# Kernel optimization log

Hardware: AMD Instinct MI355X
Metric: run time of the kernel (lower is better)

Reference implementation:

```python
import jax, jax.numpy as jnp
import numpy as np

NUM_HEADS = 6
HEAD_SIZE = 64
N_EMBD = 384


def setup_inputs() -> dict:
    key = jax.random.key(0)
    ks = jax.random.split(key, 6)
    B, T, C = 4, 2048, N_EMBD
    D = NUM_HEADS * HEAD_SIZE  # 384
    x = jax.random.normal(ks[0], (B, T, C), dtype=jnp.float32)
    scale = 1.0 / np.sqrt(C)
    Wq = jax.random.normal(ks[1], (C, D), dtype=jnp.float32) * scale
    Wk = jax.random.normal(ks[2], (C, D), dtype=jnp.float32) * scale
    Wv = jax.random.normal(ks[3], (C, D), dtype=jnp.float32) * scale
    Wp = jax.random.normal(ks[4], (D, N_EMBD), dtype=jnp.float32) * scale
    bp = jnp.zeros((N_EMBD,), dtype=jnp.float32)
    return {"x": x, "Wq": Wq, "Wk": Wk, "Wv": Wv, "Wp": Wp, "bp": bp}


def reference(x, Wq, Wk, Wv, Wp, bp):
    B, T, C = x.shape
    H, Dh = NUM_HEADS, HEAD_SIZE
    # QKV projections (no bias), split into heads: [B, H, T, Dh]
    q = (x @ Wq).reshape(B, T, H, Dh).transpose(0, 2, 1, 3)
    k = (x @ Wk).reshape(B, T, H, Dh).transpose(0, 2, 1, 3)
    v = (x @ Wv).reshape(B, T, H, Dh).transpose(0, 2, 1, 3)
    # scaled dot-product scores [B, H, T, T]
    scores = jnp.einsum("bhqd,bhkd->bhqk", q, k) / jnp.sqrt(jnp.float32(Dh))
    causal = jnp.tril(jnp.ones((T, T), dtype=bool))
    scores = jnp.where(causal, scores, jnp.float32(-1e9))
    attn = jax.nn.softmax(scores, axis=-1)
    # dropout is identity at inference (Keras Dropout inactive outside training)
    out = jnp.einsum("bhqk,bhkd->bhqd", attn, v)
    out = out.transpose(0, 2, 1, 3).reshape(B, T, H * Dh)
    return out @ Wp + bp
```

## Files before the change

kernel.cpp:

```cpp
#include <hip/hip_runtime.h>
#include <hip/hip_bf16.h>

typedef __bf16 bf16x8 __attribute__((ext_vector_type(8)));
typedef float floatx4 __attribute__((ext_vector_type(4)));
typedef unsigned short us4 __attribute__((ext_vector_type(4)));
typedef unsigned short us8 __attribute__((ext_vector_type(8)));
typedef unsigned short ushort_t;

#define MFMA(a,b,c) __builtin_amdgcn_mfma_f32_16x16x32_bf16((a),(b),(c),0,0,0)


__device__ __forceinline__ ushort_t f2bf(float f){
  unsigned u = __builtin_bit_cast(unsigned, f);
  u = u + 0x7fffu + ((u>>16)&1u);
  return (ushort_t)(u>>16);
}

__device__ __forceinline__ us4 pack4(float4 a){
  us4 o;
  o[0]=f2bf(a.x); o[1]=f2bf(a.y); o[2]=f2bf(a.z); o[3]=f2bf(a.w);
  return o;
}

__device__ __forceinline__ us4 cvt4(floatx4 v){
  union { us4 s; __hip_bfloat162 h[2]; } u;
  float2 t;
  t.x=v[0]; t.y=v[1]; u.h[0]=__float22bfloat162_rn(t);
  t.x=v[2]; t.y=v[3]; u.h[1]=__float22bfloat162_rn(t);
  return u.s;
}

__global__ __launch_bounds__(256) void prep(
    const float* __restrict__ x,
    const float* __restrict__ w0, const float* __restrict__ w1,
    const float* __restrict__ w2, const float* __restrict__ w3,
    ushort_t* __restrict__ xb,
    ushort_t* __restrict__ wt_qkv, ushort_t* __restrict__ wt_p){
  __shared__ ushort_t tile[64][65];
  int bx = blockIdx.x;
  if (bx < 3072){
    int i = (bx*256 + threadIdx.x)*4;
    int row = i/384, col = i - row*384;
    float4 v = *(const float4*)(x + i);
    us4 o;
    o[0]=f2bf(v.x); o[1]=f2bf(v.y); o[2]=f2bf(v.z); o[3]=f2bf(v.w);
    *(us4*)(xb + ((row>>4)*48 + (col>>3))*128 + (row&15)*8 + (col&7)) = o;
    return;
  }
  int t6 = bx - 3072;
  int z = t6/36, rem = t6%36, by = rem/6, bxx = rem%6;
  const float* src; ushort_t* dst;
  if      (z==0){ src=w0; dst=wt_qkv;             }
  else if (z==1){ src=w1; dst=wt_qkv + 147456;    }
  else if (z==2){ src=w2; dst=wt_qkv + 2*147456;  }
  else          { src=w3; dst=wt_p;               }
  int r0 = by*64, c0 = bxx*64;
  int t = threadIdx.x, r = t>>2, cs = (t&3)*16;
  #pragma unroll
  for (int i=0;i<16;i++) tile[r][cs+i] = f2bf(src[(r0+r)*384 + c0+cs+i]);
  __syncthreads();
  int n = c0 + r, t16n = n>>4, rn = n&15;
  int k0 = r0 + cs;
  #pragma unroll
  for (int i=0;i<16;i++){
    int k = k0 + i;
    dst[(t16n*48 + (k>>3))*128 + rn*8 + (k&7)] = tile[cs+i][r];
  }
}

__global__ __launch_bounds__(64) void qkv_gemm(
    const ushort_t* __restrict__ x, const ushort_t* __restrict__ wt,
    ushort_t* __restrict__ qb, ushort_t* __restrict__ kb, ushort_t* __restrict__ vtb){
  __shared__ ushort_t tr[16*72];
  int lane = threadIdx.x&63, l15 = lane&15, quad = lane>>4;
  int mb = blockIdx.x*64, mt = blockIdx.x*4;
  int z  = blockIdx.y/6;
  int nt16 = (blockIdx.y - z*6)*4;
  int n0 = nt16*16;
  const ushort_t* wbase = wt + z*147456;
  floatx4 acc[4][4];
  #pragma unroll
  for (int qs=0;qs<4;qs++)
    #pragma unroll
    for (int nt=0;nt<4;nt++) acc[qs][nt]=(floatx4){0,0,0,0};
  #pragma unroll
  for (int kt=0; kt<12; kt++){
    bf16x8 a[4], b[4];
    #pragma unroll
    for (int qs=0; qs<4; qs++)
      a[qs] = *(const bf16x8*)(x + ((mt+qs)*48 + kt*4+quad)*128 + l15*8);
    #pragma unroll
    for (int nt=0; nt<4; nt++)
      b[nt] = *(const bf16x8*)(wbase + ((nt16+nt)*48 + kt*4+quad)*128 + l15*8);
    #pragma unroll
    for (int qs=0; qs<4; qs++)
      #pragma unroll
      for (int nt=0; nt<4; nt++)
        acc[qs][nt] = MFMA(a[qs], b[nt], acc[qs][nt]);
  }
  int h = n0>>6;
  if (z == 2){
    #pragma unroll
    for (int qs=0; qs<4; qs++){
      int rbase = mb + qs*16 + quad*4;
      int b_ = rbase >> 11, rr = rbase & 2047;
      int ct = rr>>3, e0 = rr&7;
      #pragma unroll
      for (int nt=0; nt<4; nt++){
        float4 v; v.x=acc[qs][nt][0]; v.y=acc[qs][nt][1];
                  v.z=acc[qs][nt][2]; v.w=acc[qs][nt][3];
        *(us4*)(vtb + ((b_*6+h)*1024 + nt*256 + ct)*128 + l15*8 + e0) = pack4(v);
      }
    }
  } else {
    float qscale = (z==0) ? 0.18033688011112042f : 1.0f;
    ushort_t* dstp = (z==0) ? qb : kb;
    #pragma unroll
    for (int qs=0; qs<4; qs++){
      int rbase = mb + qs*16;
      int b_ = rbase>>11, t16 = (rbase&2047)>>4;
      #pragma unroll
      for (int nt=0; nt<4; nt++)
        #pragma unroll
        for (int j=0; j<4; j++)
          tr[(quad*4+j)*72 + nt*16 + l15] = f2bf(acc[qs][nt][j]*qscale);
      us8 v0 = *(const us8*)(&tr[l15*72 + quad*8]);
      us8 v1 = *(const us8*)(&tr[l15*72 + (quad+4)*8]);
      int hbase = (b_*6+h)*1024 + t16*8;
      *(us8*)(dstp + (hbase + quad  )*128 + l15*8) = v0;
      *(us8*)(dstp + (hbase + quad+4)*128 + l15*8) = v1;
    }
  }
}

__device__ __forceinline__ void subtile(
    const bf16x8 (&kf)[4][2], const bf16x8 (&vf)[4][2], bf16x8 ones,
    bf16x8 qf0, bf16x8 qf1,
    floatx4 (&o4)[4], floatx4& lsum,
    ushort_t* pwv, int qg, int kv0, bool diag, int l15, int quad){
  floatx4 s[4];
  #pragma unroll
  for (int nt=0; nt<4; nt++){
    floatx4 z = {0,0,0,0};
    z = MFMA(kf[nt][0], qf0, z);
    z = MFMA(kf[nt][1], qf1, z);
    s[nt] = z;
  }
  ushort_t* prow = pwv + l15*72;
  if (diag){
    #pragma unroll
    for (int nt=0; nt<4; nt++){
      floatx4 p;
      #pragma unroll
      for (int r=0;r<4;r++){
        int kvg = kv0 + nt*16 + quad*4 + r;
        float sv = (kvg > qg) ? -1e30f : s[nt][r];
        p[r] = exp2f(sv);
      }
      *(us4*)(prow + nt*16 + quad*4) = cvt4(p);
    }
  } else {
    #pragma unroll
    for (int nt=0; nt<4; nt++){
      floatx4 p;
      #pragma unroll
      for (int r=0;r<4;r++) p[r] = exp2f(s[nt][r]);
      *(us4*)(prow + nt*16 + quad*4) = cvt4(p);
    }
  }
  bf16x8 pa0 = *(const bf16x8*)(prow + quad*8);
  bf16x8 pa1 = *(const bf16x8*)(prow + 32 + quad*8);
  #pragma unroll
  for (int nt=0; nt<4; nt++){
    o4[nt] = MFMA(pa0, vf[nt][0], o4[nt]);
    o4[nt] = MFMA(pa1, vf[nt][1], o4[nt]);
  }
  lsum = MFMA(pa0, ones, lsum);
  lsum = MFMA(pa1, ones, lsum);
}

__global__ __launch_bounds__(256,2) void attn(
    const ushort_t* __restrict__ qb, const ushort_t* __restrict__ kb,
    const ushort_t* __restrict__ vtb, ushort_t* __restrict__ ob){
  __shared__ float smem[4608];
  int bx = blockIdx.x;
  int hb = bx % 24;
  int p  = bx / 24;
  int tA = p, tB = 63 - p;
  int ktA = tA >> 1, ktB = tB >> 1;
  int h = hb % 6, b = hb / 6;
  int lane = threadIdx.x&63, w = threadIdx.x>>6, l15 = lane&15, quad = lane>>4;
  const ushort_t* qbase = qb  + (b*6+h)*131072;
  const ushort_t* kbase = kb  + (b*6+h)*131072;
  const ushort_t* vbase = vtb + (b*6+h)*131072;

  bf16x8 qfA[2][2], qfB[2][2];
  #pragma unroll
  for (int s=0; s<2; s++){
    const ushort_t* qpA = qbase + ((tA*2+s)*8 + quad)*128 + l15*8;
    qfA[s][0] = *(const bf16x8*)(qpA);
    qfA[s][1] = *(const bf16x8*)(qpA + 512);
    const ushort_t* qpB = qbase + ((tB*2+s)*8 + quad)*128 + l15*8;
    qfB[s][0] = *(const bf16x8*)(qpB);
    qfB[s][1] = *(const bf16x8*)(qpB + 512);
  }
  union { us8 u; bf16x8 v; } onesu;
  #pragma unroll
  for (int i=0;i<8;i++) onesu.u[i] = 0x3F80;
  bf16x8 ones = onesu.v;

  floatx4 oA[2][4], oB[2][4];
  floatx4 lsA[2], lsB[2];
  #pragma unroll
  for (int s=0;s<2;s++){
    lsA[s] = (floatx4){0,0,0,0};
    lsB[s] = (floatx4){0,0,0,0};
    #pragma unroll
    for (int i=0;i<4;i++){ oA[s][i]=(floatx4){0,0,0,0}; oB[s][i]=(floatx4){0,0,0,0}; }
  }

  ushort_t* pw = (ushort_t*)smem + w*1152;
  int qA0 = tA*32, qB0 = tB*32;

  for (int kt=w; kt<=ktB; kt+=4){
    int kv0 = kt*64;
    bf16x8 kf[4][2], vf[4][2];
    #pragma unroll
    for (int nt=0; nt<4; nt++){
      const ushort_t* kp = kbase + ((kt*4+nt)*8 + quad)*128 + l15*8;
      kf[nt][0] = *(const bf16x8*)(kp);
      kf[nt][1] = *(const bf16x8*)(kp + 512);
      const ushort_t* vp = vbase + (nt*256 + kt*8 + quad)*128 + l15*8;
      vf[nt][0] = *(const bf16x8*)(vp);
      vf[nt][1] = *(const bf16x8*)(vp + 512);
    }
    bool diagB = (kt == ktB);
    subtile(kf,vf,ones,qfB[0][0],qfB[0][1], oB[0], lsB[0], pw, qB0   +l15, kv0, diagB, l15, quad);
    subtile(kf,vf,ones,qfB[1][0],qfB[1][1], oB[1], lsB[1], pw, qB0+16+l15, kv0, diagB, l15, quad);
    if (kt <= ktA){
      bool diagA = (kt == ktA);
      subtile(kf,vf,ones,qfA[0][0],qfA[0][1], oA[0], lsA[0], pw, qA0   +l15, kv0, diagA, l15, quad);
      subtile(kf,vf,ones,qfA[1][0],qfA[1][1], oA[1], lsA[1], pw, qA0+16+l15, kv0, diagA, l15, quad);
    }
  }

  float* lsh = smem + 4352;
  if (l15==0){
    #pragma unroll
    for (int j=0;j<4;j++){
      lsh[w*64 +      quad*4 + j] = lsA[0][j];
      lsh[w*64 + 16 + quad*4 + j] = lsA[1][j];
      lsh[w*64 + 32 + quad*4 + j] = lsB[0][j];
      lsh[w*64 + 48 + quad*4 + j] = lsB[1][j];
    }
  }

  auto do_chunk = [&](const floatx4 (&oc)[4], int c, int grc){
    __syncthreads();
    #pragma unroll
    for (int j=0;j<4;j++){
      int r16 = quad*4 + j;
      #pragma unroll
      for (int nt=0;nt<4;nt++)
        smem[w*1088 + r16*68 + nt*16 + l15] = oc[nt][j];
    }
    __syncthreads();
    #pragma unroll
    for (int jj=0;jj<4;jj++){
      int r16 = w*4 + jj;
      float l = lsh[c*16+r16] + lsh[64+c*16+r16]
              + lsh[128+c*16+r16] + lsh[192+c*16+r16];
      float acc = smem[r16*68+lane] + smem[1088 + r16*68+lane]
                + smem[2176 + r16*68+lane] + smem[3264 + r16*68+lane];
      ob[((b*128 + grc)*48 + h*8 + (lane>>3))*128 + r16*8 + (lane&7)]
          = f2bf(acc/l);
    }
  };
  do_chunk(oA[0], 0, tA*2);
  do_chunk(oA[1], 1, tA*2+1);
  do_chunk(oB[0], 2, tB*2);
  do_chunk(oB[1], 3, tB*2+1);
}

__global__ __launch_bounds__(64) void proj_gemm(
    const ushort_t* __restrict__ a, const ushort_t* __restrict__ wpt,
    const float* __restrict__ bp, float* __restrict__ out){
  int lane = threadIdx.x&63, l15 = lane&15, quad = lane>>4;
  int mb = blockIdx.x*64, mt = blockIdx.x*4;
  int nb = blockIdx.y*64, nt16 = blockIdx.y*4;
  floatx4 acc[4][4];
  #pragma unroll
  for (int qs=0;qs<4;qs++)
    #pragma unroll
    for (int nt=0;nt<4;nt++) acc[qs][nt]=(floatx4){0,0,0,0};
  #pragma unroll
  for (int kt=0; kt<12; kt++){
    bf16x8 av[4], bv[4];
    #pragma unroll
    for (int qs=0; qs<4; qs++)
      av[qs] = *(const bf16x8*)(a + ((mt+qs)*48 + kt*4+quad)*128 + l15*8);
    #pragma unroll
    for (int nt=0; nt<4; nt++)
      bv[nt] = *(const bf16x8*)(wpt + ((nt16+nt)*48 + kt*4+quad)*128 + l15*8);
    #pragma unroll
    for (int qs=0; qs<4; qs++)
      #pragma unroll
      for (int nt=0; nt<4; nt++)
        acc[qs][nt] = MFMA(av[qs], bv[nt], acc[qs][nt]);
  }
  #pragma unroll
  for (int qs=0; qs<4; qs++){
    #pragma unroll
    for (int nt=0; nt<4; nt++){
      int c = nb + nt*16 + l15;
      float bias = bp[c];
      #pragma unroll
      for (int j=0; j<4; j++){
        int r = mb + qs*16 + quad*4 + j;
        out[r*384 + c] = acc[qs][nt][j] + bias;
      }
    }
  }
}

extern "C" void kernel_launch(void* const* d_in, const int* in_sizes, int n_in,
                              void* d_out, int out_size, void* d_ws, size_t ws_size,
                              hipStream_t stream){
  const float* x  = (const float*)d_in[0];
  const float* Wq = (const float*)d_in[1];
  const float* Wk = (const float*)d_in[2];
  const float* Wv = (const float*)d_in[3];
  const float* Wp = (const float*)d_in[4];
  const float* bp = (const float*)d_in[5];
  float* out = (float*)d_out;

  ushort_t* xb  = (ushort_t*)d_ws;
  ushort_t* wt  = xb  + 8192*384;
  ushort_t* wpt = wt  + 1152*384;
  ushort_t* qb  = wpt + 384*384;
  ushort_t* kb  = qb  + 8192*384;
  ushort_t* vtb = kb  + 8192*384;
  ushort_t* ab  = vtb + 8192*384;

  prep     <<<dim3(3216),   256, 0, stream>>>(x,Wq,Wk,Wv,Wp,xb,wt,wpt);
  qkv_gemm <<<dim3(128,18), 64,  0, stream>>>(xb, wt, qb, kb, vtb);
  attn     <<<dim3(768),    256, 0, stream>>>(qb, kb, vtb, ab);
  proj_gemm<<<dim3(128,6),  64,  0, stream>>>(ab, wpt, bp, out);
}
```

Measured before the change: 132.8 us.

## Prefetch next K/V tile and interleave score/PV stages across subtiles

Splits the per-subtile work into separate score and PV phases using four LDS probability slices per wave, so score MFMAs for one query subtile can overlap PV MFMAs of another. K and V fragments for the next kv tile are loaded into registers during the current iteration (software pipelining) to hide global memory latency. This quadruples per-wave LDS staging and adds register pressure from double-buffered fragments, which may reduce occupancy or cause spills.

Result: no change. 131.5 us, median of 3 (-1.0%).

```diff
diff --git a/kernel.cpp b/kernel.cpp
--- a/kernel.cpp
+++ b/kernel.cpp
@@ -133,11 +133,9 @@
   }
 }
 
-__device__ __forceinline__ void subtile(
-    const bf16x8 (&kf)[4][2], const bf16x8 (&vf)[4][2], bf16x8 ones,
-    bf16x8 qf0, bf16x8 qf1,
-    floatx4 (&o4)[4], floatx4& lsum,
-    ushort_t* pwv, int qg, int kv0, bool diag, int l15, int quad){
+__device__ __forceinline__ void score(
+    const bf16x8 (&kf)[4][2], bf16x8 qf0, bf16x8 qf1,
+    ushort_t* slice, int qg, int kv0, bool diag, int l15, int quad){
   floatx4 s[4];
   #pragma unroll
   for (int nt=0; nt<4; nt++){
@@ -146,7 +144,7 @@
     z = MFMA(kf[nt][1], qf1, z);
     s[nt] = z;
   }
-  ushort_t* prow = pwv + l15*72;
+  ushort_t* prow = slice + l15*72;
   if (diag){
     #pragma unroll
     for (int nt=0; nt<4; nt++){
@@ -168,6 +166,12 @@
       *(us4*)(prow + nt*16 + quad*4) = cvt4(p);
     }
   }
+}
+
+__device__ __forceinline__ void pv(
+    const bf16x8 (&vf)[4][2], bf16x8 ones, ushort_t* slice,
+    floatx4 (&o4)[4], floatx4& lsum, int l15, int quad){
+  ushort_t* prow = slice + l15*72;
   bf16x8 pa0 = *(const bf16x8*)(prow + quad*8);
   bf16x8 pa1 = *(const bf16x8*)(prow + 32 + quad*8);
   #pragma unroll
@@ -182,7 +186,7 @@
 __global__ __launch_bounds__(256,2) void attn(
     const ushort_t* __restrict__ qb, const ushort_t* __restrict__ kb,
     const ushort_t* __restrict__ vtb, ushort_t* __restrict__ ob){
-  __shared__ float smem[4608];
+  __shared__ float smem[9472];
   int bx = blockIdx.x;
   int hb = bx % 24;
   int p  = bx / 24;
@@ -219,32 +223,62 @@
     for (int i=0;i<4;i++){ oA[s][i]=(floatx4){0,0,0,0}; oB[s][i]=(floatx4){0,0,0,0}; }
   }
 
-  ushort_t* pw = (ushort_t*)smem + w*1152;
+  ushort_t* s0 = (ushort_t*)smem + w*4608;
+  ushort_t* s1 = s0 + 1152;
+  ushort_t* s2 = s0 + 2304;
+  ushort_t* s3 = s0 + 3456;
   int qA0 = tA*32, qB0 = tB*32;
+
+  auto LOADK = [&](int t, bf16x8 (&kf_)[4][2]){
+    #pragma unroll
+    for (int nt=0; nt<4; nt++){
+      const ushort_t* kp = kbase + ((t*4+nt)*8 + quad)*128 + l15*8;
+      kf_[nt][0] = *(const bf16x8*)(kp);
+      kf_[nt][1] = *(const bf16x8*)(kp + 512);
+    }
+  };
+  auto LOADV = [&](int t, bf16x8 (&vf_)[4][2]){
+    #pragma unroll
+    for (int nt=0; nt<4; nt++){
+      const ushort_t* vp = vbase + (nt*256 + t*8 + quad)*128 + l15*8;
+      vf_[nt][0] = *(const bf16x8*)(vp);
+      vf_[nt][1] = *(const bf16x8*)(vp + 512);
+    }
+  };
+
+  bf16x8 kf[4][2], vf[4][2];
+  LOADK(w, kf); LOADV(w, vf);
 
   for (int kt=w; kt<=ktB; kt+=4){
     int kv0 = kt*64;
-    bf16x8 kf[4][2], vf[4][2];
-    #pragma unroll
-    for (int nt=0; nt<4; nt++){
-      const ushort_t* kp = kbase + ((kt*4+nt)*8 + quad)*128 + l15*8;
-      kf[nt][0] = *(const bf16x8*)(kp);
-      kf[nt][1] = *(const bf16x8*)(kp + 512);
-      const ushort_t* vp = vbase + (nt*256 + kt*8 + quad)*128 + l15*8;
-      vf[nt][0] = *(const bf16x8*)(vp);
-      vf[nt][1] = *(const bf16x8*)(vp + 512);
-    }
+    int ktn = (kt+4 <= ktB) ? kt+4 : ktB;
     bool diagB = (kt == ktB);
-    subtile(kf,vf,ones,qfB[0][0],qfB[0][1], oB[0], lsB[0], pw, qB0   +l15, kv0, diagB, l15, quad);
-    subtile(kf,vf,ones,qfB[1][0],qfB[1][1], oB[1], lsB[1], pw, qB0+16+l15, kv0, diagB, l15, quad);
+    bf16x8 kn[4][2], vn[4][2];
+    score(kf, qfB[0][0],qfB[0][1], s0, qB0   +l15, kv0, diagB, l15, quad);
+    score(kf, qfB[1][0],qfB[1][1], s1, qB0+16+l15, kv0, diagB, l15, quad);
+    pv(vf, ones, s0, oB[0], lsB[0], l15, quad);
     if (kt <= ktA){
       bool diagA = (kt == ktA);
-      subtile(kf,vf,ones,qfA[0][0],qfA[0][1], oA[0], lsA[0], pw, qA0   +l15, kv0, diagA, l15, quad);
-      subtile(kf,vf,ones,qfA[1][0],qfA[1][1], oA[1], lsA[1], pw, qA0+16+l15, kv0, diagA, l15, quad);
-    }
-  }
-
-  float* lsh = smem + 4352;
+      score(kf, qfA[0][0],qfA[0][1], s2, qA0   +l15, kv0, diagA, l15, quad);
+      pv(vf, ones, s1, oB[1], lsB[1], l15, quad);
+      score(kf, qfA[1][0],qfA[1][1], s3, qA0+16+l15, kv0, diagA, l15, quad);
+      LOADK(ktn, kn);
+      pv(vf, ones, s2, oA[0], lsA[0], l15, quad);
+      pv(vf, ones, s3, oA[1], lsA[1], l15, quad);
+      LOADV(ktn, vn);
+    } else {
+      pv(vf, ones, s1, oB[1], lsB[1], l15, quad);
+      LOADK(ktn, kn);
+      LOADV(ktn, vn);
+    }
+    #pragma unroll
+    for (int nt=0; nt<4; nt++){
+      kf[nt][0]=kn[nt][0]; kf[nt][1]=kn[nt][1];
+      vf[nt][0]=vn[nt][0]; vf[nt][1]=vn[nt][1];
+    }
+  }
+
+  float* lsh = smem + 9216;
   if (l15==0){
     #pragma unroll
     for (int j=0;j<4;j++){
```

## Give each attention block one query tile and split score/PV into separate stages

Applied to the files above, without the earlier changes.

Before, each attention block handled a pair of query tiles (p and 63-p) to balance the causal workload. Now each block handles a single 32-row query tile, the grid doubles to 1536 blocks, and blocks are ordered from the longest tile to the shortest. The per-subtile routine is split into a score step and a PV step, and each 16-row half gets its own LDS slice so both score computations can be issued before the PV MFMAs, giving the scheduler more independent work. The cost is that K/V fragments are loaded twice as often across the grid, per-block work is uneven, and LDS use per block grows.

After: 131.9 us. No clear change (-0.6%).

```diff
diff --git a/kernel.cpp b/kernel.cpp
--- a/kernel.cpp
+++ b/kernel.cpp
@@ -133,11 +133,9 @@
   }
 }
 
-__device__ __forceinline__ void subtile(
-    const bf16x8 (&kf)[4][2], const bf16x8 (&vf)[4][2], bf16x8 ones,
-    bf16x8 qf0, bf16x8 qf1,
-    floatx4 (&o4)[4], floatx4& lsum,
-    ushort_t* pwv, int qg, int kv0, bool diag, int l15, int quad){
+__device__ __forceinline__ void score(
+    const bf16x8 (&kf)[4][2], bf16x8 qf0, bf16x8 qf1,
+    ushort_t* slice, int qg, int kv0, bool diag, int l15, int quad){
   floatx4 s[4];
   #pragma unroll
   for (int nt=0; nt<4; nt++){
@@ -146,7 +144,7 @@
     z = MFMA(kf[nt][1], qf1, z);
     s[nt] = z;
   }
-  ushort_t* prow = pwv + l15*72;
+  ushort_t* prow = slice + l15*72;
   if (diag){
     #pragma unroll
     for (int nt=0; nt<4; nt++){
@@ -168,6 +166,12 @@
       *(us4*)(prow + nt*16 + quad*4) = cvt4(p);
     }
   }
+}
+
+__device__ __forceinline__ void pv(
+    const bf16x8 (&vf)[4][2], bf16x8 ones, ushort_t* slice,
+    floatx4 (&o4)[4], floatx4& lsum, int l15, int quad){
+  ushort_t* prow = slice + l15*72;
   bf16x8 pa0 = *(const bf16x8*)(prow + quad*8);
   bf16x8 pa1 = *(const bf16x8*)(prow + 32 + quad*8);
   #pragma unroll
@@ -182,49 +186,46 @@
 __global__ __launch_bounds__(256,2) void attn(
     const ushort_t* __restrict__ qb, const ushort_t* __restrict__ kb,
     const ushort_t* __restrict__ vtb, ushort_t* __restrict__ ob){
-  __shared__ float smem[4608];
+  __shared__ float smem[4736];
   int bx = blockIdx.x;
   int hb = bx % 24;
-  int p  = bx / 24;
-  int tA = p, tB = 63 - p;
-  int ktA = tA >> 1, ktB = tB >> 1;
+  int ti = bx / 24;
+  int t  = 63 - ti;
+  int ktm = t >> 1;
   int h = hb % 6, b = hb / 6;
   int lane = threadIdx.x&63, w = threadIdx.x>>6, l15 = lane&15, quad = lane>>4;
   const ushort_t* qbase = qb  + (b*6+h)*131072;
   const ushort_t* kbase = kb  + (b*6+h)*131072;
   const ushort_t* vbase = vtb + (b*6+h)*131072;
 
-  bf16x8 qfA[2][2], qfB[2][2];
+  bf16x8 qf[2][2];
   #pragma unroll
   for (int s=0; s<2; s++){
-    const ushort_t* qpA = qbase + ((tA*2+s)*8 + quad)*128 + l15*8;
-    qfA[s][0] = *(const bf16x8*)(qpA);
-    qfA[s][1] = *(const bf16x8*)(qpA + 512);
-    const ushort_t* qpB = qbase + ((tB*2+s)*8 + quad)*128 + l15*8;
-    qfB[s][0] = *(const bf16x8*)(qpB);
-    qfB[s][1] = *(const bf16x8*)(qpB + 512);
+    const ushort_t* qp = qbase + ((t*2+s)*8 + quad)*128 + l15*8;
+    qf[s][0] = *(const bf16x8*)(qp);
+    qf[s][1] = *(const bf16x8*)(qp + 512);
   }
   union { us8 u; bf16x8 v; } onesu;
   #pragma unroll
   for (int i=0;i<8;i++) onesu.u[i] = 0x3F80;
   bf16x8 ones = onesu.v;
 
-  floatx4 oA[2][4], oB[2][4];
-  floatx4 lsA[2], lsB[2];
+  floatx4 o[2][4];
+  floatx4 ls[2];
   #pragma unroll
   for (int s=0;s<2;s++){
-    lsA[s] = (floatx4){0,0,0,0};
-    lsB[s] = (floatx4){0,0,0,0};
-    #pragma unroll
-    for (int i=0;i<4;i++){ oA[s][i]=(floatx4){0,0,0,0}; oB[s][i]=(floatx4){0,0,0,0}; }
-  }
-
-  ushort_t* pw = (ushort_t*)smem + w*1152;
-  int qA0 = tA*32, qB0 = tB*32;
-
-  for (int kt=w; kt<=ktB; kt+=4){
+    ls[s] = (floatx4){0,0,0,0};
+    #pragma unroll
+    for (int i=0;i<4;i++) o[s][i]=(floatx4){0,0,0,0};
+  }
+
+  ushort_t* s0 = (ushort_t*)smem + w*2304;
+  ushort_t* s1 = s0 + 1152;
+  int q0 = t*32;
+
+  bf16x8 kf[4][2], vf[4][2];
+  for (int kt=w; kt<=ktm; kt+=4){
     int kv0 = kt*64;
-    bf16x8 kf[4][2], vf[4][2];
     #pragma unroll
     for (int nt=0; nt<4; nt++){
       const ushort_t* kp = kbase + ((kt*4+nt)*8 + quad)*128 + l15*8;
@@ -234,24 +235,19 @@
       vf[nt][0] = *(const bf16x8*)(vp);
       vf[nt][1] = *(const bf16x8*)(vp + 512);
     }
-    bool diagB = (kt == ktB);
-    subtile(kf,vf,ones,qfB[0][0],qfB[0][1], oB[0], lsB[0], pw, qB0   +l15, kv0, diagB, l15, quad);
-    subtile(kf,vf,ones,qfB[1][0],qfB[1][1], oB[1], lsB[1], pw, qB0+16+l15, kv0, diagB, l15, quad);
-    if (kt <= ktA){
-      bool diagA = (kt == ktA);
-      subtile(kf,vf,ones,qfA[0][0],qfA[0][1], oA[0], lsA[0], pw, qA0   +l15, kv0, diagA, l15, quad);
-      subtile(kf,vf,ones,qfA[1][0],qfA[1][1], oA[1], lsA[1], pw, qA0+16+l15, kv0, diagA, l15, quad);
-    }
-  }
-
-  float* lsh = smem + 4352;
+    bool diag = (kt == ktm);
+    score(kf, qf[0][0],qf[0][1], s0, q0   +l15, kv0, diag, l15, quad);
+    score(kf, qf[1][0],qf[1][1], s1, q0+16+l15, kv0, diag, l15, quad);
+    pv(vf, ones, s0, o[0], ls[0], l15, quad);
+    pv(vf, ones, s1, o[1], ls[1], l15, quad);
+  }
+
+  float* lsh = smem + 4608;
   if (l15==0){
     #pragma unroll
     for (int j=0;j<4;j++){
-      lsh[w*64 +      quad*4 + j] = lsA[0][j];
-      lsh[w*64 + 16 + quad*4 + j] = lsA[1][j];
-      lsh[w*64 + 32 + quad*4 + j] = lsB[0][j];
-      lsh[w*64 + 48 + quad*4 + j] = lsB[1][j];
+      lsh[w*32 +      quad*4 + j] = ls[0][j];
+      lsh[w*32 + 16 + quad*4 + j] = ls[1][j];
     }
   }
 
@@ -268,18 +264,16 @@
     #pragma unroll
     for (int jj=0;jj<4;jj++){
       int r16 = w*4 + jj;
-      float l = lsh[c*16+r16] + lsh[64+c*16+r16]
-              + lsh[128+c*16+r16] + lsh[192+c*16+r16];
+      float l = lsh[c*16+r16] + lsh[32+c*16+r16]
+              + lsh[64+c*16+r16] + lsh[96+c*16+r16];
       float acc = smem[r16*68+lane] + smem[1088 + r16*68+lane]
                 + smem[2176 + r16*68+lane] + smem[3264 + r16*68+lane];
       ob[((b*128 + grc)*48 + h*8 + (lane>>3))*128 + r16*8 + (lane&7)]
           = f2bf(acc/l);
     }
   };
-  do_chunk(oA[0], 0, tA*2);
-  do_chunk(oA[1], 1, tA*2+1);
-  do_chunk(oB[0], 2, tB*2);
-  do_chunk(oB[1], 3, tB*2+1);
+  do_chunk(o[0], 0, t*2);
+  do_chunk(o[1], 1, t*2+1);
 }
 
 __global__ __launch_bounds__(64) void proj_gemm(
@@ -344,6 +338,6 @@
 
   prep     <<<dim3(3216),   256, 0, stream>>>(x,Wq,Wk,Wv,Wp,xb,wt,wpt);
   qkv_gemm <<<dim3(128,18), 64,  0, stream>>>(xb, wt, qb, kb, vtb);
-  attn     <<<dim3(768),    256, 0, stream>>>(qb, kb, vtb, ab);
+  attn     <<<dim3(1536),   256, 0, stream>>>(qb, kb, vtb, ab);
   proj_gemm<<<dim3(128,6),  64,  0, stream>>>(ab, wpt, bp, out);
 }
```
